# Optimization experiments

Hardware: AMD Instinct MI355X
Metric: run time of the kernel (lower is better)

Reference implementation:

```python
import jax, jax.numpy as jnp
import numpy as np

NUM_NODES = 8192
IN_FEATURES = 1024
OUT_FEATURES = 512
NUM_EDGES = 262144  # avg degree 32


def setup_inputs() -> dict:
    key = jax.random.key(0)
    k_x, k_w, k_b, k_src, k_dst = jax.random.split(key, 5)
    x = jax.random.normal(k_x, (NUM_NODES, IN_FEATURES), dtype=jnp.float32)
    # torch nn.Linear layout: weight [out, in], bias [out]
    W = jax.random.normal(k_w, (OUT_FEATURES, IN_FEATURES), dtype=jnp.float32) * (1.0 / np.sqrt(IN_FEATURES))
    b = jax.random.normal(k_b, (OUT_FEATURES,), dtype=jnp.float32) * 0.01
    src = jax.random.randint(k_src, (NUM_EDGES,), 0, NUM_NODES, dtype=jnp.int64)
    dst = jax.random.randint(k_dst, (NUM_EDGES,), 0, NUM_NODES, dtype=jnp.int64)
    edge_index = jnp.stack([src, dst], axis=0)
    return {"x": x, "W": W, "b": b, "edge_index": edge_index, "num_nodes": NUM_NODES}


def reference(x, W, b, edge_index, num_nodes):
    # Faithful to the torch module: build dense adjacency from edge list
    # (duplicate edges collapse to 1.0 via assignment semantics),
    # linear, (dropout p=0 -> identity), dense adj @ hidden, relu.
    adj = jnp.zeros((num_nodes, num_nodes), dtype=x.dtype)
    adj = adj.at[edge_index[0], edge_index[1]].set(1.0)
    hidden = x @ W.T + b            # [N, out]
    support = adj @ hidden          # [N, out] aggregation over neighbors
    return jax.nn.relu(support)
```

## Files before the change

### kernel.cpp

```cpp
#include <hip/hip_runtime.h>

#define N_NODES 8192
#define IN_F    1024
#define OUT_F   512
#define N_EDGES 262144
#define STRIDE  96

#define HID_OFF     0u
#define XB_OFF      8388608u
#define WB_OFF      25165824u
#define DEG_OFF     26214400u
#define COL_OFF     26247168u
#define MAX_DEG     STRIDE

typedef short  bf16x8 __attribute__((ext_vector_type(8)));
typedef float  f32x4  __attribute__((ext_vector_type(4)));

__device__ __forceinline__ unsigned short f2bf(float f) {
    unsigned u = __float_as_uint(f);
    u += 0x7fffu + ((u >> 16) & 1u);
    return (unsigned short)(u >> 16);
}

__device__ __forceinline__ float bflo(unsigned u) { return __uint_as_float(u << 16); }
__device__ __forceinline__ float bfhi(unsigned u) { return __uint_as_float(u & 0xffff0000u); }

__device__ __forceinline__ void ld_lds16(const void* g, void* l) {
    __builtin_amdgcn_global_load_lds(
        (const __attribute__((address_space(1))) void*)g,
        (__attribute__((address_space(3))) void*)l, 16, 0, 0);
}

#define NX8 (N_NODES * IN_F / 8)
#define NW8 (OUT_F * IN_F / 8)
__global__ __launch_bounds__(256) void cvt_bf16_all(const float* __restrict__ x,
                                                    const float* __restrict__ w,
                                                    unsigned short* __restrict__ xb,
                                                    int* __restrict__ deg) {
    int i = blockIdx.x * blockDim.x + threadIdx.x;
    if (i < N_NODES) deg[i] = 0;
    if (i >= NX8 + NW8) return;
    const f32x4* p = (i < NX8) ? ((const f32x4*)x + (size_t)i * 2)
                               : ((const f32x4*)w + (size_t)(i - NX8) * 2);
    f32x4 v0 = __builtin_nontemporal_load(p);
    f32x4 v1 = __builtin_nontemporal_load(p + 1);
    uint4 o;
    o.x = (unsigned)f2bf(v0.x) | ((unsigned)f2bf(v0.y) << 16);
    o.y = (unsigned)f2bf(v0.z) | ((unsigned)f2bf(v0.w) << 16);
    o.z = (unsigned)f2bf(v1.x) | ((unsigned)f2bf(v1.y) << 16);
    o.w = (unsigned)f2bf(v1.z) | ((unsigned)f2bf(v1.w) << 16);
    *((uint4*)xb + i) = o;
}

__global__ __launch_bounds__(256, 6) void gemm_scatter(const unsigned short* __restrict__ Xb,
                                                       const unsigned short* __restrict__ Wb,
                                                       const float* __restrict__ bias,
                                                       unsigned short* __restrict__ H,
                                                       const int* __restrict__ src,
                                                       const int* __restrict__ dst,
                                                       int* __restrict__ deg,
                                                       int* __restrict__ col) {
    __shared__ unsigned short As[64 * 64];
    __shared__ unsigned short Bs[64 * 64];

    const int bid = blockIdx.x;
    const int tid = threadIdx.x;

    if (bid >= 1024) {
        int e = (bid - 1024) * 256 + tid;
        int s = src[e];
        int slot = atomicAdd(&deg[s], 1);
        if (slot < STRIDE) col[s * STRIDE + slot] = dst[e];
        return;
    }

    const int lane = tid & 63;
    const int wave = tid >> 6;
    const int row0 = (bid & 127) * 64;
    const int col0 = (bid >> 7) * 64;
    const int wm   = (wave & 1) * 32;
    const int wn   = (wave >> 1) * 32;
    const int fm   = lane & 15;
    const int fm7  = fm & 7;
    const int q    = lane >> 4;

    f32x4 acc[2][2];
#pragma unroll
    for (int i = 0; i < 2; ++i)
#pragma unroll
        for (int j = 0; j < 2; ++j) acc[i][j] = (f32x4)0.f;

    const int r0 = tid >> 3;
    const int kp = ((tid & 7) ^ (r0 & 7)) * 8;

    for (int k0 = 0; k0 < IN_F; k0 += 64) {
        ld_lds16(Xb + (size_t)(row0 + r0) * IN_F + k0 + kp,      As + tid * 8);
        ld_lds16(Xb + (size_t)(row0 + r0 + 32) * IN_F + k0 + kp, As + (tid + 256) * 8);
        ld_lds16(Wb + (size_t)(col0 + r0) * IN_F + k0 + kp,      Bs + tid * 8);
        ld_lds16(Wb + (size_t)(col0 + r0 + 32) * IN_F + k0 + kp, Bs + (tid + 256) * 8);
        __syncthreads();

#pragma unroll
        for (int s = 0; s < 2; ++s) {
            const int kq = s * 4 + q;
            bf16x8 a[2], b[2];
#pragma unroll
            for (int mi = 0; mi < 2; ++mi)
                a[mi] = *(const bf16x8*)&As[(((wm + mi * 16 + fm) << 3) + (kq ^ fm7)) << 3];
#pragma unroll
            for (int ni = 0; ni < 2; ++ni)
                b[ni] = *(const bf16x8*)&Bs[(((wn + ni * 16 + fm) << 3) + (kq ^ fm7)) << 3];
#pragma unroll
            for (int mi = 0; mi < 2; ++mi)
#pragma unroll
                for (int ni = 0; ni < 2; ++ni)
                    acc[mi][ni] = __builtin_amdgcn_mfma_f32_16x16x32_bf16(
                        a[mi], b[ni], acc[mi][ni], 0, 0, 0);
        }
        __syncthreads();
    }

    const int cm = (lane >> 4) * 4;
#pragma unroll
    for (int ni = 0; ni < 2; ++ni) {
        const int c = col0 + wn + ni * 16 + fm;
        const float bv = bias[c];
#pragma unroll
        for (int mi = 0; mi < 2; ++mi) {
#pragma unroll
            for (int r = 0; r < 4; ++r) {
                const int row = row0 + wm + mi * 16 + cm + r;
                H[(size_t)row * OUT_F + c] = f2bf(acc[mi][ni][r] + bv);
            }
        }
    }
}

__global__ __launch_bounds__(256) void aggregate(const unsigned short* __restrict__ H,
                                                 const int* __restrict__ dg,
                                                 const int* __restrict__ col,
                                                 float* __restrict__ out) {
    __shared__ int nbr[4][MAX_DEG];
    __shared__ int uniq[4][MAX_DEG];
    __shared__ int wcnt[4];
    const int wave = threadIdx.x >> 6;
    const int lane = threadIdx.x & 63;
    const int v    = blockIdx.x * 4 + wave;
    int d = dg[v];
    if (d > MAX_DEG) d = MAX_DEG;

    if (lane == 0) wcnt[wave] = 0;
    int id0 = -1, id1 = -1;
    if (lane < d)      { id0 = col[v * STRIDE + lane];      nbr[wave][lane]      = id0; }
    if (64 + lane < d) { id1 = col[v * STRIDE + 64 + lane]; nbr[wave][64 + lane] = id1; }
    __builtin_amdgcn_wave_barrier();

    bool k0 = (lane < d);
    const int lim0 = k0 ? lane : 0;
    for (int j = 0; j < lim0; ++j) k0 = k0 & (nbr[wave][j] != id0);
    bool k1 = (64 + lane < d);
    const int lim1 = k1 ? (64 + lane) : 0;
    for (int j = 0; j < lim1; ++j) k1 = k1 & (nbr[wave][j] != id1);
    if (k0) uniq[wave][atomicAdd(&wcnt[wave], 1)] = id0;
    if (k1) uniq[wave][atomicAdd(&wcnt[wave], 1)] = id1;
    __builtin_amdgcn_wave_barrier();
    const int n  = wcnt[wave];
    const int f0 = lane * 8;

    float a0=0,a1=0,a2=0,a3=0,a4=0,a5=0,a6=0,a7=0;
    int e = 0;
    for (; e + 4 <= n; e += 4) {
        const int i0 = uniq[wave][e], i1 = uniq[wave][e+1],
                  i2 = uniq[wave][e+2], i3 = uniq[wave][e+3];
        uint4 h0 = *(const uint4*)&H[(size_t)i0 * OUT_F + f0];
        uint4 h1 = *(const uint4*)&H[(size_t)i1 * OUT_F + f0];
        uint4 h2 = *(const uint4*)&H[(size_t)i2 * OUT_F + f0];
        uint4 h3 = *(const uint4*)&H[(size_t)i3 * OUT_F + f0];
        a0 += bflo(h0.x)+bflo(h1.x)+bflo(h2.x)+bflo(h3.x);
        a1 += bfhi(h0.x)+bfhi(h1.x)+bfhi(h2.x)+bfhi(h3.x);
        a2 += bflo(h0.y)+bflo(h1.y)+bflo(h2.y)+bflo(h3.y);
        a3 += bfhi(h0.y)+bfhi(h1.y)+bfhi(h2.y)+bfhi(h3.y);
        a4 += bflo(h0.z)+bflo(h1.z)+bflo(h2.z)+bflo(h3.z);
        a5 += bfhi(h0.z)+bfhi(h1.z)+bfhi(h2.z)+bfhi(h3.z);
        a6 += bflo(h0.w)+bflo(h1.w)+bflo(h2.w)+bflo(h3.w);
        a7 += bfhi(h0.w)+bfhi(h1.w)+bfhi(h2.w)+bfhi(h3.w);
    }
    for (; e < n; ++e) {
        uint4 h0 = *(const uint4*)&H[(size_t)uniq[wave][e] * OUT_F + f0];
        a0 += bflo(h0.x); a1 += bfhi(h0.x);
        a2 += bflo(h0.y); a3 += bfhi(h0.y);
        a4 += bflo(h0.z); a5 += bfhi(h0.z);
        a6 += bflo(h0.w); a7 += bfhi(h0.w);
    }
    f32x4 o0 = {fmaxf(a0,0.f), fmaxf(a1,0.f), fmaxf(a2,0.f), fmaxf(a3,0.f)};
    f32x4 o1 = {fmaxf(a4,0.f), fmaxf(a5,0.f), fmaxf(a6,0.f), fmaxf(a7,0.f)};
    __builtin_nontemporal_store(o0, (f32x4*)&out[(size_t)v * OUT_F + f0]);
    __builtin_nontemporal_store(o1, (f32x4*)&out[(size_t)v * OUT_F + f0 + 4]);
}

extern "C" void kernel_launch(void* const* d_in, const int* in_sizes, int n_in,
                              void* d_out, int out_size, void* d_ws, size_t ws_size,
                              hipStream_t stream) {
    const float* x  = (const float*)d_in[0];
    const float* W  = (const float*)d_in[1];
    const float* b  = (const float*)d_in[2];
    const int*   ei = (const int*)d_in[3];
    float* out = (float*)d_out;

    char* ws = (char*)d_ws;
    unsigned short* H   = (unsigned short*)(ws + HID_OFF);
    unsigned short* Xb  = (unsigned short*)(ws + XB_OFF);
    unsigned short* Wb  = (unsigned short*)(ws + WB_OFF);
    int*            deg = (int*)(ws + DEG_OFF);
    int*            col = (int*)(ws + COL_OFF);

    cvt_bf16_all<<<(NX8 + NW8 + 255) / 256, 256, 0, stream>>>(x, W, Xb, deg);

    gemm_scatter<<<2048, 256, 0, stream>>>(Xb, Wb, b, H, ei, ei + N_EDGES, deg, col);

    aggregate<<<N_NODES / 4, 256, 0, stream>>>(H, deg, col, out);
}
```

Before: 139.2 us.

## Fuse X fp32-to-bf16 conversion into GEMM tile loads

Stops converting the whole X matrix to bf16 in a separate pre-pass and staging it through workspace. The GEMM now reads fp32 X directly, converts it in registers and writes the swizzled bf16 tile to LDS, while W still goes through the async global-to-LDS path. This drops a full 32MB read plus 16MB write-and-reread of X. In exchange, each GEMM block reads twice as many bytes for X, and these loads now go through registers on the synchronous path. With 8 column blocks per row tile, X is fetched from fp32 repeatedly, though mostly from L2.

```diff
diff --git a/kernel.cpp b/kernel.cpp
--- a/kernel.cpp
+++ b/kernel.cpp
@@ -7,19 +7,18 @@
 #define STRIDE  96
 
 #define HID_OFF     0u
-#define XB_OFF      8388608u
-#define WB_OFF      25165824u
-#define DEG_OFF     26214400u
-#define COL_OFF     26247168u
+#define WB_OFF      8388608u
+#define DEG_OFF     9437184u
+#define COL_OFF     9469952u
 #define MAX_DEG     STRIDE
 
 typedef short  bf16x8 __attribute__((ext_vector_type(8)));
 typedef float  f32x4  __attribute__((ext_vector_type(4)));
 
-__device__ __forceinline__ unsigned short f2bf(float f) {
+__device__ __forceinline__ unsigned f2bf(float f) {
     unsigned u = __float_as_uint(f);
     u += 0x7fffu + ((u >> 16) & 1u);
-    return (unsigned short)(u >> 16);
+    return u >> 16;
 }
 
 __device__ __forceinline__ float bflo(unsigned u) { return __uint_as_float(u << 16); }
@@ -31,28 +30,24 @@
         (__attribute__((address_space(3))) void*)l, 16, 0, 0);
 }
 
-#define NX8 (N_NODES * IN_F / 8)
 #define NW8 (OUT_F * IN_F / 8)
-__global__ __launch_bounds__(256) void cvt_bf16_all(const float* __restrict__ x,
-                                                    const float* __restrict__ w,
-                                                    unsigned short* __restrict__ xb,
-                                                    int* __restrict__ deg) {
+__global__ __launch_bounds__(256) void prep(const float* __restrict__ w,
+                                            unsigned short* __restrict__ wb,
+                                            int* __restrict__ deg) {
     int i = blockIdx.x * blockDim.x + threadIdx.x;
     if (i < N_NODES) deg[i] = 0;
-    if (i >= NX8 + NW8) return;
-    const f32x4* p = (i < NX8) ? ((const f32x4*)x + (size_t)i * 2)
-                               : ((const f32x4*)w + (size_t)(i - NX8) * 2);
+    const f32x4* p = (const f32x4*)w + (size_t)i * 2;
     f32x4 v0 = __builtin_nontemporal_load(p);
     f32x4 v1 = __builtin_nontemporal_load(p + 1);
     uint4 o;
-    o.x = (unsigned)f2bf(v0.x) | ((unsigned)f2bf(v0.y) << 16);
-    o.y = (unsigned)f2bf(v0.z) | ((unsigned)f2bf(v0.w) << 16);
-    o.z = (unsigned)f2bf(v1.x) | ((unsigned)f2bf(v1.y) << 16);
-    o.w = (unsigned)f2bf(v1.z) | ((unsigned)f2bf(v1.w) << 16);
-    *((uint4*)xb + i) = o;
-}
-
-__global__ __launch_bounds__(256, 6) void gemm_scatter(const unsigned short* __restrict__ Xb,
+    o.x = f2bf(v0.x) | (f2bf(v0.y) << 16);
+    o.y = f2bf(v0.z) | (f2bf(v0.w) << 16);
+    o.z = f2bf(v1.x) | (f2bf(v1.y) << 16);
+    o.w = f2bf(v1.z) | (f2bf(v1.w) << 16);
+    *((uint4*)wb + i) = o;
+}
+
+__global__ __launch_bounds__(256, 6) void gemm_scatter(const float* __restrict__ X,
                                                        const unsigned short* __restrict__ Wb,
                                                        const float* __restrict__ bias,
                                                        unsigned short* __restrict__ H,
@@ -90,14 +85,32 @@
 #pragma unroll
         for (int j = 0; j < 2; ++j) acc[i][j] = (f32x4)0.f;
 
-    const int r0 = tid >> 3;
-    const int kp = ((tid & 7) ^ (r0 & 7)) * 8;
+    const int ar   = tid >> 2;
+    const int ak4  = tid & 3;
+    const int ar7  = ar & 7;
+    unsigned short* As_w0 = As + ar * 64 + ((ak4 * 2)     ^ ar7) * 8;
+    unsigned short* As_w1 = As + ar * 64 + ((ak4 * 2 + 1) ^ ar7) * 8;
+    const float* xrow = &X[(size_t)(row0 + ar) * IN_F + ak4 * 16];
+
+    const int br = tid >> 3;
+    const int bk = ((tid & 7) ^ (br & 7)) * 8;
 
     for (int k0 = 0; k0 < IN_F; k0 += 64) {
-        ld_lds16(Xb + (size_t)(row0 + r0) * IN_F + k0 + kp,      As + tid * 8);
-        ld_lds16(Xb + (size_t)(row0 + r0 + 32) * IN_F + k0 + kp, As + (tid + 256) * 8);
-        ld_lds16(Wb + (size_t)(col0 + r0) * IN_F + k0 + kp,      Bs + tid * 8);
-        ld_lds16(Wb + (size_t)(col0 + r0 + 32) * IN_F + k0 + kp, Bs + (tid + 256) * 8);
+        const f32x4* px = (const f32x4*)(xrow + k0);
+        f32x4 v0 = px[0], v1 = px[1], v2 = px[2], v3 = px[3];
+        ld_lds16(Wb + (size_t)(col0 + br) * IN_F + k0 + bk,      Bs + tid * 8);
+        ld_lds16(Wb + (size_t)(col0 + br + 32) * IN_F + k0 + bk, Bs + (tid + 256) * 8);
+        uint4 pa, pb;
+        pa.x = f2bf(v0.x) | (f2bf(v0.y) << 16);
+        pa.y = f2bf(v0.z) | (f2bf(v0.w) << 16);
+        pa.z = f2bf(v1.x) | (f2bf(v1.y) << 16);
+        pa.w = f2bf(v1.z) | (f2bf(v1.w) << 16);
+        pb.x = f2bf(v2.x) | (f2bf(v2.y) << 16);
+        pb.y = f2bf(v2.z) | (f2bf(v2.w) << 16);
+        pb.z = f2bf(v3.x) | (f2bf(v3.y) << 16);
+        pb.w = f2bf(v3.z) | (f2bf(v3.w) << 16);
+        *(uint4*)As_w0 = pa;
+        *(uint4*)As_w1 = pb;
         __syncthreads();
 
 #pragma unroll
@@ -130,7 +143,7 @@
 #pragma unroll
             for (int r = 0; r < 4; ++r) {
                 const int row = row0 + wm + mi * 16 + cm + r;
-                H[(size_t)row * OUT_F + c] = f2bf(acc[mi][ni][r] + bv);
+                H[(size_t)row * OUT_F + c] = (unsigned short)f2bf(acc[mi][ni][r] + bv);
             }
         }
     }
@@ -209,14 +222,13 @@
 
     char* ws = (char*)d_ws;
     unsigned short* H   = (unsigned short*)(ws + HID_OFF);
-    unsigned short* Xb  = (unsigned short*)(ws + XB_OFF);
     unsigned short* Wb  = (unsigned short*)(ws + WB_OFF);
     int*            deg = (int*)(ws + DEG_OFF);
     int*            col = (int*)(ws + COL_OFF);
 
-    cvt_bf16_all<<<(NX8 + NW8 + 255) / 256, 256, 0, stream>>>(x, W, Xb, deg);
-
-    gemm_scatter<<<2048, 256, 0, stream>>>(Xb, Wb, b, H, ei, ei + N_EDGES, deg, col);
+    prep<<<NW8 / 256, 256, 0, stream>>>(W, Wb, deg);
+
+    gemm_scatter<<<2048, 256, 0, stream>>>(x, Wb, b, H, ei, ei + N_EDGES, deg, col);
 
     aggregate<<<N_NODES / 4, 256, 0, stream>>>(H, deg, col, out);
 }
```

Result: no change. 141.7 us (+1.8%).
